# Performance work log

Hardware: AMD Instinct MI355X
Metric: run time of the kernel (lower is better)

Reference implementation:

```python
import jax, jax.numpy as jnp
import numpy as np


def conv3x3(x, w):
    # NCHW conv, stride 1, padding 1, no bias
    return jax.lax.conv_general_dilated(
        x, w, window_strides=(1, 1), padding=((1, 1), (1, 1)),
        dimension_numbers=('NCHW', 'OIHW', 'NCHW'))


def deform_conv2d(x, offset, w):
    """torchvision-style DeformConv2d: kernel 3x3, stride 1, pad 1, dil 1,
    1 weight group, 1 offset group, no bias.
    x: [B,C,H,W]; offset: [B,2*9,H,W] interleaved (dy,dx) per kernel tap;
    w: [O,C,3,3].
    """
    B, C, H, W = x.shape
    K = 9
    off = offset.reshape(B, K, 2, H, W)
    # kernel tap displacements relative to output pixel (pad=1 => -1..1)
    ky = jnp.repeat(jnp.arange(3) - 1, 3).astype(x.dtype)  # [9]
    kx = jnp.tile(jnp.arange(3) - 1, 3).astype(x.dtype)    # [9]
    hh = jnp.arange(H, dtype=x.dtype)
    ww = jnp.arange(W, dtype=x.dtype)
    # fractional sampling positions, [B,K,H,W]
    py = off[:, :, 0] + hh[None, None, :, None] + ky[None, :, None, None]
    px = off[:, :, 1] + ww[None, None, None, :] + kx[None, :, None, None]

    y0 = jnp.floor(py)
    x0 = jnp.floor(px)
    wy1 = py - y0
    wx1 = px - x0
    wy0 = 1.0 - wy1
    wx0 = 1.0 - wx1

    xf = x.reshape(B, C, 1, H * W)  # flatten spatial for gather

    def corner(yy, xx, wt):
        valid = (yy >= 0) & (yy <= H - 1) & (xx >= 0) & (xx <= W - 1)
        yi = jnp.clip(yy, 0, H - 1).astype(jnp.int32)
        xi = jnp.clip(xx, 0, W - 1).astype(jnp.int32)
        idx = (yi * W + xi).reshape(B, 1, K, H * W)
        v = jnp.take_along_axis(xf, idx, axis=3)  # [B,C,K,H*W]
        return v * (wt * valid.astype(x.dtype)).reshape(B, 1, K, H * W)

    samp = (corner(y0, x0, wy0 * wx0) + corner(y0, x0 + 1, wy0 * wx1)
            + corner(y0 + 1, x0, wy1 * wx0) + corner(y0 + 1, x0 + 1, wy1 * wx1))
    # samp: [B,C,K,H*W]; contract kernel taps and input channels
    out = jnp.einsum('ock,bckp->bop', w.reshape(w.shape[0], C, K), samp)
    return out.reshape(B, w.shape[0], H, W)


def setup_inputs() -> dict:
    key = jax.random.key(0)
    k1, k2, k3, k4, k5 = jax.random.split(key, 5)
    B, C, H, W = 8, 64, 128, 128
    lr = jax.random.normal(k1, (B, C, H, W), dtype=jnp.float32)
    hr = jax.random.normal(k2, (B, C, H, W), dtype=jnp.float32)
    w_est = jax.random.normal(k3, (2 * C, 2 * C, 3, 3), dtype=jnp.float32) * 0.02
    w_off = jax.random.normal(k4, (18, 2 * C, 3, 3), dtype=jnp.float32) * 0.02
    w_def = jax.random.normal(k5, (C, C, 3, 3), dtype=jnp.float32) * 0.05
    return {"lr_features": lr, "hr_features": hr,
            "w_est": w_est, "w_off": w_off, "w_def": w_def}


def reference(lr_features, hr_features, w_est, w_off, w_def):
    # concat LR/HR features -> offset estimator -> offset conv -> deform conv
    inp = jnp.concatenate((lr_features, hr_features), axis=1)  # [B,2C,H,W]
    est = jax.nn.leaky_relu(conv3x3(inp, w_est), 0.1)          # offset estimator
    offset = conv3x3(est, w_off)                                # [B,18,H,W]
    return deform_conv2d(hr_features, offset, w_def)
```

## Files before the change

### kernel.cpp

```cpp
#include <hip/hip_runtime.h>
#include <hip/hip_bf16.h>

#define BB 8
#define CC 64
#define C2 128
#define HH 128
#define WW 128
#define HW (HH * WW)

typedef __attribute__((ext_vector_type(8))) short bf16x8;
typedef __attribute__((ext_vector_type(4))) float f32x4;
typedef __attribute__((ext_vector_type(2))) float f32x2;
typedef __attribute__((ext_vector_type(4))) unsigned u32x4;

__device__ inline ushort f2bf(float f) {
    union { float f; unsigned u; } v; v.f = f;
    unsigned r = v.u + 0x7fff + ((v.u >> 16) & 1);
    return (ushort)(r >> 16);
}
__device__ inline float bf2f(ushort u) {
    union { unsigned u; float f; } v; v.u = (unsigned)u << 16; return v.f;
}

__global__ __launch_bounds__(256) void to_nhwc_bf16(
    const float* __restrict__ lr, const float* __restrict__ hr,
    ushort* __restrict__ dst) {
    __shared__ ushort lt[HH][136];
    const int t = threadIdx.x;
    const int b = blockIdx.x >> 7, y = blockIdx.x & 127;
    for (int ci0 = 0; ci0 < 128; ci0 += 2) {
        const int ci = ci0 + (t >> 7);
        const int x = t & 127;
        const float* s = (ci < 64) ? lr + ((size_t)(b * 64 + ci)) * HW
                                   : hr + ((size_t)(b * 64 + ci - 64)) * HW;
        lt[x][ci] = f2bf(s[y * WW + x]);
    }
    __syncthreads();
    ushort* db = dst + ((size_t)blockIdx.x) * WW * 128;
    for (int i = t; i < 128 * 16; i += 256) {
        const int px = i >> 4, q = i & 15;
        uint4 v = *(const uint4*)&lt[px][q * 8];
        *(uint4*)&db[(size_t)px * 128 + q * 8] = v;
    }
}

__global__ void pack_all(const float* __restrict__ wE, const float* __restrict__ wO,
                         const float* __restrict__ wD, ushort* __restrict__ oE,
                         ushort* __restrict__ oO, ushort* __restrict__ oD,
                         ushort* __restrict__ zp) {
    int i = blockIdx.x * 256 + threadIdx.x;
    if (i < 147456) {
        int c7 = i & 7, co = (i >> 3) & 127, kb = i >> 10;
        int lg = kb & 3, ct = kb >> 2, tap = ct % 9, cc = ct / 9;
        int ci = cc * 32 + lg * 8 + c7;
        oE[i] = f2bf(wE[((size_t)co * 128 + ci) * 9 + tap]);
        return;
    }
    i -= 147456;
    if (i < 36864) {
        int c7 = i & 7, co = (i >> 3) & 31, kb = i >> 8;
        int lg = kb & 3, ct = kb >> 2, tap = ct % 9, cc = ct / 9;
        int ci = cc * 32 + lg * 8 + c7;
        oO[i] = (co < 18) ? f2bf(wO[((size_t)co * 128 + ci) * 9 + tap]) : (ushort)0;
        return;
    }
    i -= 36864;
    if (i < 36864) {
        int c7 = i & 7, co = (i >> 3) & 63, lg = (i >> 9) & 3, h = (i >> 11) & 1,
            tap = i >> 12;
        int c = h * 32 + lg * 8 + c7;
        oD[i] = f2bf(wD[((size_t)co * 64 + c) * 9 + tap]);
        return;
    }
    i -= 36864;
    if (i < 128) zp[i] = 0;
}

#define SLOTS 3120
#define SLOTS_PAD 3136

__global__ __launch_bounds__(512) void conv1_mfma(
    const ushort* __restrict__ nhwc, const ushort* __restrict__ wE2,
    const ushort* __restrict__ zp, ushort* __restrict__ est) {
    __shared__ ushort lws[2][SLOTS_PAD * 8];
    const int t = threadIdx.x, lane = t & 63, wid = t >> 6;
    const int l15 = lane & 15, lg = lane >> 4;
    const int wm = wid >> 1, wn = wid & 1;
    const int bi0 = blockIdx.x;
    const int bi = (bi0 & 7) * 32 + (bi0 >> 3);
    const int b = bi >> 5, yt = bi & 31;
    const int y0 = yt * 4;
    const ushort* nb = nhwc + (size_t)(b * HH) * WW * 128;

    auto stage = [&](int cc, int bf) {
        for (int s0 = wid * 64; s0 < SLOTS; s0 += 512) {
            const int s = s0 + lane;
            const int sc = (s < SLOTS) ? s : (SLOTS - 1);
            const int plane = sc / 130, px = sc % 130;
            const int r = plane >> 2, q = plane & 3;
            const int yy = y0 + r - 1, xx = px - 1;
            const ushort* g =
                ((unsigned)yy < (unsigned)HH && (unsigned)xx < (unsigned)WW)
                    ? nb + ((size_t)yy * WW + xx) * 128 + cc * 32 + q * 8
                    : zp;
            __builtin_amdgcn_global_load_lds(
                (const __attribute__((address_space(1))) void*)g,
                (__attribute__((address_space(3))) void*)(&lws[bf][s0 * 8]),
                16, 0, 0);
        }
    };

    f32x4 acc[8][4] = {};
    stage(0, 0);
    __syncthreads();
#pragma unroll
    for (int cc = 0; cc < 4; ++cc) {
        if (cc < 3) stage(cc + 1, (cc + 1) & 1);
        const ushort* buf = lws[cc & 1];
#pragma unroll
        for (int tap = 0; tap < 9; ++tap) {
            const int ky = tap / 3, kx = tap % 3;
            bf16x8 a[8], w[4];
#pragma unroll
            for (int mt = 0; mt < 8; ++mt)
                a[mt] = *(const bf16x8*)
                    &buf[(((wm + ky) * 4 + lg) * 130 + mt * 16 + l15 + kx) * 8];
#pragma unroll
            for (int nt = 0; nt < 4; ++nt)
                w[nt] = *(const bf16x8*)&wE2[(size_t)(((cc * 9 + tap) * 4 + lg) * 128
                                                     + wn * 64 + nt * 16 + l15) * 8];
#pragma unroll
            for (int mt = 0; mt < 8; ++mt)
#pragma unroll
                for (int nt = 0; nt < 4; ++nt)
                    acc[mt][nt] = __builtin_amdgcn_mfma_f32_16x16x32_bf16(
                        a[mt], w[nt], acc[mt][nt], 0, 0, 0);
        }
        __syncthreads();
    }

    const int y = y0 + wm;
    ushort* eb = est + ((size_t)(b * HH + y)) * WW * 128;
#pragma unroll
    for (int mt = 0; mt < 8; ++mt)
#pragma unroll
        for (int nt = 0; nt < 4; ++nt)
#pragma unroll
            for (int j = 0; j < 4; ++j) {
                float r = acc[mt][nt][j];
                r = (r >= 0.f) ? r : 0.1f * r;
                eb[(size_t)(mt * 16 + lg * 4 + j) * 128
                   + wn * 64 + nt * 16 + l15] = f2bf(r);
            }
}

__global__ __launch_bounds__(512) void conv2_mfma(
    const ushort* __restrict__ est, const ushort* __restrict__ wO2,
    const ushort* __restrict__ zp, float* __restrict__ offs) {
    __shared__ ushort lws[2][SLOTS_PAD * 8];
    const int t = threadIdx.x, lane = t & 63, wid = t >> 6;
    const int l15 = lane & 15, lg = lane >> 4;
    const int wm = wid >> 1, wn = wid & 1;
    const int bi0 = blockIdx.x;
    const int bi = (bi0 & 7) * 32 + (bi0 >> 3);
    const int b = bi >> 5, yt = bi & 31;
    const int y0 = yt * 4;
    const ushort* nb = est + (size_t)(b * HH) * WW * 128;

    auto stage = [&](int cc, int bf) {
        for (int s0 = wid * 64; s0 < SLOTS; s0 += 512) {
            const int s = s0 + lane;
            const int sc = (s < SLOTS) ? s : (SLOTS - 1);
            const int plane = sc / 130, px = sc % 130;
            const int r = plane >> 2, q = plane & 3;
            const int yy = y0 + r - 1, xx = px - 1;
            const ushort* g =
                ((unsigned)yy < (unsigned)HH && (unsigned)xx < (unsigned)WW)
                    ? nb + ((size_t)yy * WW + xx) * 128 + cc * 32 + q * 8
                    : zp;
            __builtin_amdgcn_global_load_lds(
                (const __attribute__((address_space(1))) void*)g,
                (__attribute__((address_space(3))) void*)(&lws[bf][s0 * 8]),
                16, 0, 0);
        }
    };

    f32x4 acc[2][4] = {};
    stage(0, 0);
    __syncthreads();
#pragma unroll
    for (int cc = 0; cc < 4; ++cc) {
        if (cc < 3) stage(cc + 1, (cc + 1) & 1);
        const ushort* buf = lws[cc & 1];
#pragma unroll
        for (int tap = 0; tap < 9; ++tap) {
            const int ky = tap / 3, kx = tap % 3;
            bf16x8 aw[2], bx[4];
#pragma unroll
            for (int mt = 0; mt < 2; ++mt)
                aw[mt] = *(const bf16x8*)&wO2[(size_t)(((cc * 9 + tap) * 4 + lg) * 32
                                                      + mt * 16 + l15) * 8];
#pragma unroll
            for (int nt = 0; nt < 4; ++nt)
                bx[nt] = *(const bf16x8*)
                    &buf[(((wm + ky) * 4 + lg) * 130
                          + wn * 64 + nt * 16 + l15 + kx) * 8];
#pragma unroll
            for (int mt = 0; mt < 2; ++mt)
#pragma unroll
                for (int nt = 0; nt < 4; ++nt)
                    acc[mt][nt] = __builtin_amdgcn_mfma_f32_16x16x32_bf16(
                        aw[mt], bx[nt], acc[mt][nt], 0, 0, 0);
        }
        __syncthreads();
    }

    const int y = y0 + wm;
    float* obp = offs + (size_t)b * 18 * HW + (size_t)y * WW;
#pragma unroll
    for (int mt = 0; mt < 2; ++mt)
#pragma unroll
        for (int j = 0; j < 4; ++j) {
            const int co = mt * 16 + lg * 4 + j;
            if (co < 18)
#pragma unroll
                for (int nt = 0; nt < 4; ++nt)
                    obp[(size_t)co * HW + wn * 64 + nt * 16 + l15] = acc[mt][nt][j];
        }
}

__device__ inline void def_coords(const ushort* __restrict__ nb, int y, int x,
                                  int k, float dy, float dx, int chan_base,
                                  float* __restrict__ w,
                                  const ushort** __restrict__ p) {
    const int ky = k / 3 - 1, kx = k % 3 - 1;
    const float py  = (float)(y + ky) + dy;
    const float pxf = (float)(x + kx) + dx;
    const float y0f = floorf(py), x0f = floorf(pxf);
    const float wy1 = py - y0f, wx1 = pxf - x0f;
    const float wy0 = 1.f - wy1, wx0 = 1.f - wx1;
    const int y0 = (int)y0f, x0 = (int)x0f;
    const int y1 = y0 + 1, x1 = x0 + 1;
    const bool vy0 = (unsigned)y0 < (unsigned)HH;
    const bool vy1 = (unsigned)y1 < (unsigned)HH;
    const bool vx0 = (unsigned)x0 < (unsigned)WW;
    const bool vx1 = (unsigned)x1 < (unsigned)WW;
    w[0] = wy0 * wx0 * ((vy0 && vx0) ? 1.f : 0.f);
    w[1] = wy0 * wx1 * ((vy0 && vx1) ? 1.f : 0.f);
    w[2] = wy1 * wx0 * ((vy1 && vx0) ? 1.f : 0.f);
    w[3] = wy1 * wx1 * ((vy1 && vx1) ? 1.f : 0.f);
    const int y0c = min(max(y0, 0), HH - 1), y1c = min(max(y1, 0), HH - 1);
    const int x0c = min(max(x0, 0), WW - 1), x1c = min(max(x1, 0), WW - 1);
    p[0] = nb + ((size_t)y0c * WW + x0c) * 128 + chan_base;
    p[1] = nb + ((size_t)y0c * WW + x1c) * 128 + chan_base;
    p[2] = nb + ((size_t)y1c * WW + x0c) * 128 + chan_base;
    p[3] = nb + ((size_t)y1c * WW + x1c) * 128 + chan_base;
}

__global__ __launch_bounds__(512) void deform_mfma(
    const ushort* __restrict__ nhwc,
    const float* __restrict__ offs,
    const ushort* __restrict__ wD4,
    float* __restrict__ out) {
    __shared__ ushort wlds[9 * 4096];
    const int t = threadIdx.x, lane = t & 63, wid = t >> 6;
    const int l15 = lane & 15, lg = lane >> 4;
    const int pg = lane >> 2, q = lane & 3;
    const int bi0 = blockIdx.x;
    const int bi = (bi0 & 7) * 128 + (bi0 >> 3);
    const int xh = bi & 1, yp = (bi >> 1) & 63, b = bi >> 7;
    const int y  = yp * 2 + (wid >> 2);
    const int xo = xh * 64 + (wid & 3) * 16 + l15;
    const int xl = xh * 64 + (wid & 3) * 16 + pg;

    const ushort* nb = nhwc + (size_t)(b * HH) * WW * 128;
    const float* obl = offs + (size_t)b * 18 * HW + (size_t)y * WW + xl;
    const int cbl = 64 + q * 8;
    const int shfl_src = (l15 << 2) | lg;

#pragma unroll
    for (int i = 0; i < 9; ++i) {
        const ushort* src = wD4 + i * 4096 + (wid * 64 + lane) * 8;
        __builtin_amdgcn_global_load_lds(
            (const __attribute__((address_space(1))) void*)src,
            (__attribute__((address_space(3))) void*)(&wlds[i * 4096 + wid * 512]),
            16, 0, 0);
    }

    float dyv[9], dxv[9];
#pragma unroll
    for (int k = 0; k < 9; ++k) {
        dyv[k] = obl[(size_t)(2 * k) * HW];
        dxv[k] = obl[(size_t)(2 * k + 1) * HW];
    }
    __syncthreads();

    auto issue_g = [&](int k, u32x4* g, float* wz) {
        const ushort* p[4];
        def_coords(nb, y, xl, k, dyv[k], dxv[k], cbl, wz, p);
#pragma unroll
        for (int c = 0; c < 4; ++c) {
            asm volatile("global_load_dwordx4 %0, %1, off"
                         : "=v"(g[c]) : "v"(p[c]));
            asm volatile("global_load_dwordx4 %0, %1, off offset:64"
                         : "=v"(g[4 + c]) : "v"(p[c]));
        }
    };

    u32x4 gcur[8], gnxt[8];
    float wcur[4], wnxt[4];
    issue_g(0, gcur, wcur);

    f32x4 acc[4] = {};
#pragma unroll
    for (int k = 0; k < 9; ++k) {
        asm volatile("s_waitcnt vmcnt(0)" ::: "memory");
        __builtin_amdgcn_sched_barrier(0);
        if (k < 8) issue_g(k + 1, gnxt, wnxt);
#pragma unroll
        for (int h = 0; h < 2; ++h) {
            bf16x8 afr[4];
#pragma unroll
            for (int mt = 0; mt < 4; ++mt)
                afr[mt] = *(const bf16x8*)
                    &wlds[(size_t)(((k * 2 + h) * 4 + lg) * 64 + mt * 16 + l15) * 8];
            union { unsigned u[4]; bf16x8 v; } bv;
#pragma unroll
            for (int qq = 0; qq < 4; ++qq) {
                f32x2 s = {0.f, 0.f};
#pragma unroll
                for (int c = 0; c < 4; ++c) {
                    const unsigned u = gcur[h * 4 + c][qq];
                    f32x2 cf;
                    cf.x = __uint_as_float(u << 16);
                    cf.y = __uint_as_float(u & 0xffff0000u);
                    s.x = fmaf(wcur[c], cf.x, s.x);
                    s.y = fmaf(wcur[c], cf.y, s.y);
                }
                __hip_bfloat162 hh = __float22bfloat162_rn(make_float2(s.x, s.y));
                unsigned up; __builtin_memcpy(&up, &hh, 4);
                bv.u[qq] = (unsigned)__shfl((int)up, shfl_src);
            }
#pragma unroll
            for (int mt = 0; mt < 4; ++mt)
                acc[mt] = __builtin_amdgcn_mfma_f32_16x16x32_bf16(
                    afr[mt], bv.v, acc[mt], 0, 0, 0);
        }
#pragma unroll
        for (int c = 0; c < 8; ++c) gcur[c] = gnxt[c];
#pragma unroll
        for (int c = 0; c < 4; ++c) wcur[c] = wnxt[c];
    }

#pragma unroll
    for (int mt = 0; mt < 4; ++mt)
#pragma unroll
        for (int j = 0; j < 4; ++j) {
            const int co = mt * 16 + lg * 4 + j;
            out[(((size_t)(b * CC + co)) * HH + y) * WW + xo] = acc[mt][j];
        }
}

extern "C" void kernel_launch(void* const* d_in, const int* in_sizes, int n_in,
                              void* d_out, int out_size, void* d_ws, size_t ws_size,
                              hipStream_t stream) {
    const float* lr    = (const float*)d_in[0];
    const float* hr    = (const float*)d_in[1];
    const float* w_est = (const float*)d_in[2];
    const float* w_off = (const float*)d_in[3];
    const float* w_def = (const float*)d_in[4];
    float* out = (float*)d_out;

    char* ws = (char*)d_ws;
    ushort* in_nhwc  = (ushort*)ws;   ws += (size_t)BB * HH * WW * 128 * 2;
    ushort* est_nhwc = (ushort*)ws;   ws += (size_t)BB * HH * WW * 128 * 2;
    float*  offs     = (float*)ws;    ws += (size_t)BB * 18 * HW * 4;
    ushort* wE2      = (ushort*)ws;   ws += (size_t)128 * 1152 * 2;
    ushort* wO2      = (ushort*)ws;   ws += (size_t)144 * 32 * 8 * 2;
    ushort* wD4      = (ushort*)ws;   ws += (size_t)9 * 4096 * 2;
    ushort* zp       = (ushort*)ws;

    const int pack_total = 147456 + 36864 + 36864 + 128;
    pack_all<<<(pack_total + 255) / 256, 256, 0, stream>>>(
        w_est, w_off, w_def, wE2, wO2, wD4, zp);

    to_nhwc_bf16<<<BB * HH, 256, 0, stream>>>(lr, hr, in_nhwc);

    conv1_mfma<<<BB * (HH / 4), 512, 0, stream>>>(in_nhwc, wE2, zp, est_nhwc);
    conv2_mfma<<<BB * (HH / 4), 512, 0, stream>>>(est_nhwc, wO2, zp, offs);

    deform_mfma<<<BB * HH, 512, 0, stream>>>(in_nhwc, offs, wD4, out);
}
```

Measured before the change: 121.2 us.

## Triple-buffer LDS staging in conv kernels with one barrier per stage

Both MFMA conv kernels move from double to triple LDS buffers. The per-stage pair of __syncthreads becomes a single s_barrier, preceded by a partial vmcnt wait that lets the prefetch of the next channel chunk stay in flight while the current chunk is consumed. The goal is to cut barrier stalls and hide global-to-LDS load latency. In exchange LDS use per block rises by about half, and the hand-counted vmcnt values (7 for wave 0, 6 for the rest) depend on exactly how many loads each wave issues.

Measured after the change: 122.9 us. Within noise of the previous version (+1.4%).

```diff
diff --git a/kernel.cpp b/kernel.cpp
--- a/kernel.cpp
+++ b/kernel.cpp
@@ -82,7 +82,7 @@
 __global__ __launch_bounds__(512) void conv1_mfma(
     const ushort* __restrict__ nhwc, const ushort* __restrict__ wE2,
     const ushort* __restrict__ zp, ushort* __restrict__ est) {
-    __shared__ ushort lws[2][SLOTS_PAD * 8];
+    __shared__ ushort lws[3][SLOTS_PAD * 8];
     const int t = threadIdx.x, lane = t & 63, wid = t >> 6;
     const int l15 = lane & 15, lg = lane >> 4;
     const int wm = wid >> 1, wn = wid & 1;
@@ -112,11 +112,20 @@
 
     f32x4 acc[8][4] = {};
     stage(0, 0);
-    __syncthreads();
 #pragma unroll
     for (int cc = 0; cc < 4; ++cc) {
-        if (cc < 3) stage(cc + 1, (cc + 1) & 1);
-        const ushort* buf = lws[cc & 1];
+        if (cc < 3) stage(cc + 1, (cc + 1) % 3);
+        __builtin_amdgcn_sched_barrier(0);
+        if (cc < 3) {
+            if (wid == 0) asm volatile("s_waitcnt vmcnt(7)" ::: "memory");
+            else          asm volatile("s_waitcnt vmcnt(6)" ::: "memory");
+        } else {
+            asm volatile("s_waitcnt vmcnt(0)" ::: "memory");
+        }
+        __builtin_amdgcn_sched_barrier(0);
+        __builtin_amdgcn_s_barrier();
+        __builtin_amdgcn_sched_barrier(0);
+        const ushort* buf = lws[cc % 3];
 #pragma unroll
         for (int tap = 0; tap < 9; ++tap) {
             const int ky = tap / 3, kx = tap % 3;
@@ -136,7 +145,6 @@
                     acc[mt][nt] = __builtin_amdgcn_mfma_f32_16x16x32_bf16(
                         a[mt], w[nt], acc[mt][nt], 0, 0, 0);
         }
-        __syncthreads();
     }
 
     const int y = y0 + wm;
@@ -157,7 +165,7 @@
 __global__ __launch_bounds__(512) void conv2_mfma(
     const ushort* __restrict__ est, const ushort* __restrict__ wO2,
     const ushort* __restrict__ zp, float* __restrict__ offs) {
-    __shared__ ushort lws[2][SLOTS_PAD * 8];
+    __shared__ ushort lws[3][SLOTS_PAD * 8];
     const int t = threadIdx.x, lane = t & 63, wid = t >> 6;
     const int l15 = lane & 15, lg = lane >> 4;
     const int wm = wid >> 1, wn = wid & 1;
@@ -187,11 +195,20 @@
 
     f32x4 acc[2][4] = {};
     stage(0, 0);
-    __syncthreads();
 #pragma unroll
     for (int cc = 0; cc < 4; ++cc) {
-        if (cc < 3) stage(cc + 1, (cc + 1) & 1);
-        const ushort* buf = lws[cc & 1];
+        if (cc < 3) stage(cc + 1, (cc + 1) % 3);
+        __builtin_amdgcn_sched_barrier(0);
+        if (cc < 3) {
+            if (wid == 0) asm volatile("s_waitcnt vmcnt(7)" ::: "memory");
+            else          asm volatile("s_waitcnt vmcnt(6)" ::: "memory");
+        } else {
+            asm volatile("s_waitcnt vmcnt(0)" ::: "memory");
+        }
+        __builtin_amdgcn_sched_barrier(0);
+        __builtin_amdgcn_s_barrier();
+        __builtin_amdgcn_sched_barrier(0);
+        const ushort* buf = lws[cc % 3];
 #pragma unroll
         for (int tap = 0; tap < 9; ++tap) {
             const int ky = tap / 3, kx = tap % 3;
@@ -212,7 +229,6 @@
                     acc[mt][nt] = __builtin_amdgcn_mfma_f32_16x16x32_bf16(
                         aw[mt], bx[nt], acc[mt][nt], 0, 0, 0);
         }
-        __syncthreads();
     }
 
     const int y = y0 + wm;
```
